# Performance work log

Hardware: AMD Instinct MI355X
Metric: run time of the kernel (lower is better)

Reference implementation:

```python
import jax, jax.numpy as jnp
import numpy as np
from jax import lax

MASK_RATE = 0.2
EPS = 1e-6
H, DK = 12, 64  # heads, per-head dim


def layer_norm(x, g, b):
    mu = jnp.mean(x, axis=-1, keepdims=True)
    var = jnp.mean(jnp.square(x - mu), axis=-1, keepdims=True)
    return (x - mu) * lax.rsqrt(var + EPS) * g + b


def setup_inputs() -> dict:
    key = jax.random.key(0)
    ks = jax.random.split(key, 24)
    B, T, S, D, F, L = 64, 131072, 256, 768, 3072, 2
    w = lambda k, shp: (jax.random.normal(k, shp, jnp.float32) * 0.02)
    inp = {
        "inputs": jax.random.normal(ks[0], (B, T, 1), jnp.float32),
        "randomness": jax.random.uniform(ks[1], (B * S, 3), jnp.float32),
        "perm": jax.random.permutation(ks[2], B * S).astype(jnp.int32),
        "conv_w": w(ks[3], (512, 1, D)),
        "conv_b": jnp.zeros((D,), jnp.float32),
        "pos_emb": w(ks[4], (300, D)),
        "mask_tok": w(ks[5], (D,)),
        "agg_tok": w(ks[6], (D,)),
        "wq": w(ks[7], (L, D, D)), "bq": jnp.zeros((L, D), jnp.float32),
        "wk": w(ks[8], (L, D, D)), "bk": jnp.zeros((L, D), jnp.float32),
        "wv": w(ks[9], (L, D, D)), "bv": jnp.zeros((L, D), jnp.float32),
        "wo": w(ks[10], (L, D, D)), "bo": jnp.zeros((L, D), jnp.float32),
        "ln1_g": jnp.ones((L, D), jnp.float32), "ln1_b": jnp.zeros((L, D), jnp.float32),
        "w1": w(ks[11], (L, D, F)), "b1": jnp.zeros((L, F), jnp.float32),
        "w2": w(ks[12], (L, F, D)), "b2": jnp.zeros((L, D), jnp.float32),
        "ln2_g": jnp.ones((L, D), jnp.float32), "ln2_b": jnp.zeros((L, D), jnp.float32),
    }
    return inp


def forward(inputs, randomness, perm, conv_w, conv_b, pos_emb, mask_tok, agg_tok,
            wq, bq, wk, bk, wv, bv, wo, bo, ln1_g, ln1_b, w1, b1, w2, b2, ln2_g, ln2_b):
    # waveform -> patches: Conv1D kernel=512 stride=512 valid
    x = lax.conv_general_dilated(inputs, conv_w, window_strides=(512,), padding='VALID',
                                 dimension_numbers=('NWC', 'WIO', 'NWC')) + conv_b
    B, S, D = x.shape
    embeddings = x
    # --- BERT-style random token masking (vectorized replacement of python loop) ---
    r0, r1, r2 = randomness[:, 0], randomness[:, 1], randomness[:, 2]
    sel = r0 <= MASK_RATE
    m = (sel & (r1 <= 0.8)).astype(x.dtype).reshape(B, S)
    rnd = (sel & (r1 > 0.8) & (r2 <= 0.5)).astype(x.dtype).reshape(B, S)
    nt = (sel & (r1 > 0.8) & (r2 > 0.5)).astype(x.dtype).reshape(B, S)
    flat = lax.stop_gradient(x.reshape(B * S, D))
    shuf = flat[perm].reshape(B, S, D)
    masked = (x * (1.0 - m - rnd)[:, :, None]
              + mask_tok[None, None, :] * m[:, :, None]
              + shuf * rnd[:, :, None])
    mask_pos = m + rnd + nt
    # positional embeddings + [AGG] token
    h = masked + pos_emb[:S][None, :, :]
    h = jnp.concatenate([jnp.broadcast_to(agg_tok, (B, 1, D)), h], axis=1)  # [B, S+1, D]
    scale = 1.0 / np.sqrt(DK).astype(np.float32)
    for l in range(wq.shape[0]):
        # post-norm transformer encoder layer
        q = (jnp.einsum('bsd,de->bse', h, wq[l]) + bq[l]).reshape(B, S + 1, H, DK)
        k = (jnp.einsum('bsd,de->bse', h, wk[l]) + bk[l]).reshape(B, S + 1, H, DK)
        v = (jnp.einsum('bsd,de->bse', h, wv[l]) + bv[l]).reshape(B, S + 1, H, DK)
        scores = jnp.einsum('bqhd,bkhd->bhqk', q, k) * scale
        attn = jax.nn.softmax(scores, axis=-1)
        o = jnp.einsum('bhqk,bkhd->bqhd', attn, v).reshape(B, S + 1, D)
        o = jnp.einsum('bsd,de->bse', o, wo[l]) + bo[l]
        h = layer_norm(h + o, ln1_g[l], ln1_b[l])
        f = jax.nn.gelu(jnp.einsum('bsd,df->bsf', h, w1[l]) + b1[l])
        f = jnp.einsum('bsf,fd->bsd', f, w2[l]) + b2[l]
        h = layer_norm(h + f, ln2_g[l], ln2_b[l])
    aggregated = h[:, 0, :]
    predictions = h[:, 1:, :]  # == predictions_1d (input already [B,S,D])
    return aggregated, predictions, mask_pos, embeddings


def reference(inputs, randomness, perm, conv_w, conv_b, pos_emb, mask_tok, agg_tok,
              wq, bq, wk, bk, wv, bv, wo, bo, ln1_g, ln1_b, w1, b1, w2, b2, ln2_g, ln2_b):
    return forward(inputs, randomness, perm, conv_w, conv_b, pos_emb, mask_tok, agg_tok,
                   wq, bq, wk, bk, wv, bv, wo, bo, ln1_g, ln1_b, w1, b1, w2, b2, ln2_g, ln2_b)
```

## Files before the change

### kernel.cpp

```cpp
#include <hip/hip_runtime.h>
#include <hip/hip_bf16.h>
#include <math.h>

#define BB 64
#define SS 256
#define SP 257
#define DD 768
#define FF 3072
#define HH 12
#define DKK 64
#define ROWS (BB*SP)
#define MPAD 16512
#define MCONV (BB*SS)
#define RB ((size_t)ROWS * DD)
#define PRB ((size_t)MPAD * DD)

typedef short bf16x8 __attribute__((ext_vector_type(8)));
typedef float f32x4 __attribute__((ext_vector_type(4)));
typedef unsigned short ushort8v __attribute__((ext_vector_type(8)));

__device__ __forceinline__ ushort f2bf(float x) {
    union { __hip_bfloat16 h; ushort u; } c;
    c.h = __float2bfloat16(x);
    return c.u;
}
__device__ __forceinline__ float bf2f(ushort u) {
    union { __hip_bfloat16 h; ushort u; } c;
    c.u = u;
    return __bfloat162float(c.h);
}

__device__ __forceinline__ float gelu_tanh_f(float x) {
    float x3 = x * x * x;
    float u = 0.7978845608028654f * (x + 0.044715f * x3);
    return 0.5f * x * (1.0f + tanhf(u));
}

__device__ __forceinline__ void gload16(const ushort* g, ushort* l) {
    __builtin_amdgcn_global_load_lds(
        (__attribute__((address_space(1))) void*)(g),
        (__attribute__((address_space(3))) void*)(l), 16, 0, 0);
}

template <bool IS_MAX>
__device__ __forceinline__ float blk_reduce(float v, float* red4) {
    #pragma unroll
    for (int o = 32; o > 0; o >>= 1) {
        float other = __shfl_down(v, o, 64);
        v = IS_MAX ? fmaxf(v, other) : (v + other);
    }
    __syncthreads();
    if ((threadIdx.x & 63) == 0) red4[threadIdx.x >> 6] = v;
    __syncthreads();
    if (IS_MAX) return fmaxf(fmaxf(red4[0], red4[1]), fmaxf(red4[2], red4[3]));
    return red4[0] + red4[1] + red4[2] + red4[3];
}

__global__ __launch_bounds__(256) void conv_in_bf_kernel(
    const float* __restrict__ in, ushort* __restrict__ out)
{
    const size_t i = ((size_t)blockIdx.x * 256 + threadIdx.x) * 4;
    float4 v = *reinterpret_cast<const float4*>(&in[i]);
    ushort4 o;
    o.x = f2bf(v.x); o.y = f2bf(v.y); o.z = f2bf(v.z); o.w = f2bf(v.w);
    *reinterpret_cast<ushort4*>(&out[i]) = o;
}

__global__ __launch_bounds__(256) void wt_kernel(
    const float* __restrict__ W, ushort* __restrict__ Wt, int K, int N)
{
    __shared__ float tile[32][33];
    const int k0 = blockIdx.x * 32, n0 = blockIdx.y * 32;
    const int t = threadIdx.x;
    {
        const int r = t >> 3, c4 = (t & 7) * 4;
        float4 v = *reinterpret_cast<const float4*>(&W[(size_t)(k0 + r) * N + n0 + c4]);
        tile[r][c4 + 0] = v.x; tile[r][c4 + 1] = v.y;
        tile[r][c4 + 2] = v.z; tile[r][c4 + 3] = v.w;
    }
    __syncthreads();
    {
        const int n = t >> 3, k4 = (t & 7) * 4;
        ushort4 o;
        o.x = f2bf(tile[k4 + 0][n]); o.y = f2bf(tile[k4 + 1][n]);
        o.z = f2bf(tile[k4 + 2][n]); o.w = f2bf(tile[k4 + 3][n]);
        *reinterpret_cast<ushort4*>(&Wt[(size_t)(n0 + n) * K + k0 + k4]) = o;
    }
}

template <bool C_BF16, bool GELU>
__global__ __launch_bounds__(256) void gemm128(
    const ushort* __restrict__ A, const ushort* __restrict__ Bt,
    const float* __restrict__ bias, void* __restrict__ Cp,
    int M, int N, int K)
{
    __shared__ ushort As[128 * 64];
    __shared__ ushort Bs[128 * 64];
    const int tid = threadIdx.x;
    const int lane = tid & 63, w = tid >> 6;
    const int wr = w & 1, wc = w >> 1;
    const int lg = lane >> 4, lr = lane & 15;
    const int row0 = blockIdx.y * 128, col0 = blockIdx.x * 128;

    f32x4 acc[4][4];
    #pragma unroll
    for (int m = 0; m < 4; ++m)
        #pragma unroll
        for (int n = 0; n < 4; ++n)
            acc[m][n] = (f32x4){0.f, 0.f, 0.f, 0.f};

    const int g_rowoff = w * 8 + (lane >> 3);
    const int g_colu   = (lane & 7) * 8;

    for (int k0 = 0; k0 < K; k0 += 64) {
        #pragma unroll
        for (int r = 0; r < 4; ++r) {
            const int row = r * 32 + g_rowoff;
            gload16(&A[(size_t)(row0 + row) * K + k0 + g_colu],
                    &As[r * 2048 + w * 512]);
            gload16(&Bt[(size_t)(col0 + row) * K + k0 + g_colu],
                    &Bs[r * 2048 + w * 512]);
        }
        __syncthreads();

        #pragma unroll
        for (int ks = 0; ks < 2; ++ks) {
            bf16x8 af[4], bf[4];
            #pragma unroll
            for (int m = 0; m < 4; ++m)
                af[m] = *reinterpret_cast<const bf16x8*>(
                    &As[(wr * 64 + m * 16 + lr) * 64 + ks * 32 + lg * 8]);
            #pragma unroll
            for (int n = 0; n < 4; ++n)
                bf[n] = *reinterpret_cast<const bf16x8*>(
                    &Bs[(wc * 64 + n * 16 + lr) * 64 + ks * 32 + lg * 8]);
            #pragma unroll
            for (int m = 0; m < 4; ++m)
                #pragma unroll
                for (int n = 0; n < 4; ++n)
                    acc[m][n] = __builtin_amdgcn_mfma_f32_16x16x32_bf16(
                        af[m], bf[n], acc[m][n], 0, 0, 0);
        }
        __syncthreads();
    }

    #pragma unroll
    for (int m = 0; m < 4; ++m) {
        #pragma unroll
        for (int n = 0; n < 4; ++n) {
            const int col = col0 + wc * 64 + n * 16 + lr;
            const float bcol = bias[col];
            #pragma unroll
            for (int j = 0; j < 4; ++j) {
                const int row = row0 + wr * 64 + m * 16 + lg * 4 + j;
                float v = acc[m][n][j] + bcol;
                if (GELU) v = gelu_tanh_f(v);
                if (C_BF16) ((ushort*)Cp)[(size_t)row * N + col] = f2bf(v);
                else        ((float*)Cp)[(size_t)row * N + col] = v;
            }
        }
    }
}

__global__ __launch_bounds__(256) void build_h_kernel(
    const float* __restrict__ emb, const float* __restrict__ rnd3,
    const int* __restrict__ perm, const float* __restrict__ pos_emb,
    const float* __restrict__ mask_tok, const float* __restrict__ agg_tok,
    float* __restrict__ h, ushort* __restrict__ hb, float* __restrict__ mask_pos)
{
    const int sf = blockIdx.x;
    const int b = blockIdx.y;
    const int t = threadIdx.x;
    const size_t ro = ((size_t)b * SP + sf) * DD;
    float* hrow = h + ro;
    ushort* hbrow = hb + ro;
    if (sf == 0) {
        #pragma unroll
        for (int i = 0; i < 3; ++i) {
            const float v = agg_tok[t + 256 * i];
            hrow[t + 256 * i] = v;
            hbrow[t + 256 * i] = f2bf(v);
        }
        return;
    }
    const int s = sf - 1;
    const int idx = b * SS + s;
    const float r0 = rnd3[idx * 3 + 0];
    const float r1 = rnd3[idx * 3 + 1];
    const float r2 = rnd3[idx * 3 + 2];
    const bool sel = (r0 <= 0.2f);
    const float m  = (sel && r1 <= 0.8f) ? 1.f : 0.f;
    const float rn = (sel && r1 > 0.8f && r2 <= 0.5f) ? 1.f : 0.f;
    const float nt = (sel && r1 > 0.8f && r2 > 0.5f) ? 1.f : 0.f;
    if (t == 0) mask_pos[idx] = m + rn + nt;
    const int p = perm[idx];
    const float* xrow = emb + (size_t)idx * DD;
    const float* srow = emb + (size_t)p * DD;
    const float keep = 1.f - m - rn;
    #pragma unroll
    for (int i = 0; i < 3; ++i) {
        const int c = t + 256 * i;
        const float v = xrow[c] * keep + mask_tok[c] * m + srow[c] * rn + pos_emb[s * DD + c];
        hrow[c] = v;
        hbrow[c] = f2bf(v);
    }
}

__global__ __launch_bounds__(256) void vt_kernel(
    const ushort* __restrict__ V, ushort* __restrict__ Vt)
{
    const int bh = blockIdx.x;
    const int b = bh / HH, h = bh % HH;
    const int t = threadIdx.x;
    __shared__ ushort tile[64][65];
    const size_t vtb = (size_t)bh * 64 * 288;
    const int d = t & 63, kk = t >> 6;
    const int kq = t & 63, dg = t >> 6;
    for (int kt = 0; kt < 5; ++kt) {
        #pragma unroll
        for (int i = 0; i < 16; ++i) {
            const int r = kk + 4 * i;
            const int kg = kt * 64 + r;
            tile[r][d] = (kg < SP) ? V[((size_t)b * SP + kg) * DD + h * 64 + d] : (ushort)0;
        }
        __syncthreads();
        #pragma unroll
        for (int i = 0; i < 16; ++i) {
            const int dd2 = dg + 4 * i;
            const int k = kt * 64 + kq;
            if (k < 288) Vt[vtb + (size_t)dd2 * 288 + k] = tile[kq][dd2];
        }
        __syncthreads();
    }
}

__global__ __launch_bounds__(256) void attn_mfma(
    const ushort* __restrict__ Q, const ushort* __restrict__ K,
    const ushort* __restrict__ Vt, ushort* __restrict__ O)
{
    const int h = blockIdx.x, b = blockIdx.y;
    const int t = threadIdx.x, lane = t & 63, w = t >> 6;
    const int lg = lane >> 4, lr = lane & 15;
    __shared__ ushort Pl[4][16][296];

    const size_t qkbase = ((size_t)b * SP) * DD + (size_t)h * DKK;
    const size_t vtbase = (size_t)(b * HH + h) * 64 * 288;

    #pragma unroll
    for (int i = 0; i < 4; ++i) Pl[w][lr][272 + lg * 4 + i] = 0;

    for (int p = 0; p < 5; ++p) {
        const int q0 = p * 64 + w * 16;
        const int qr = min(q0 + lr, SP - 1);
        bf16x8 aq0 = *reinterpret_cast<const bf16x8*>(&Q[qkbase + (size_t)qr * DD + lg * 8]);
        bf16x8 aq1 = *reinterpret_cast<const bf16x8*>(&Q[qkbase + (size_t)qr * DD + 32 + lg * 8]);

        f32x4 sc[17];
        #pragma unroll
        for (int n = 0; n < 17; ++n) {
            const int kr = min(n * 16 + lr, SP - 1);
            const ushort* kp = &K[qkbase + (size_t)kr * DD + lg * 8];
            bf16x8 bk0 = *reinterpret_cast<const bf16x8*>(kp);
            bf16x8 bk1 = *reinterpret_cast<const bf16x8*>(kp + 32);
            f32x4 a = (f32x4){0.f, 0.f, 0.f, 0.f};
            a = __builtin_amdgcn_mfma_f32_16x16x32_bf16(aq0, bk0, a, 0, 0, 0);
            a = __builtin_amdgcn_mfma_f32_16x16x32_bf16(aq1, bk1, a, 0, 0, 0);
            sc[n] = a;
        }

        float rmax[4] = {-1e30f, -1e30f, -1e30f, -1e30f};
        #pragma unroll
        for (int n = 0; n < 17; ++n) {
            const int kcol = n * 16 + lr;
            if (kcol >= SP) {
                sc[n] = (f32x4){-1e30f, -1e30f, -1e30f, -1e30f};
            } else {
                sc[n] *= 0.125f;
            }
            #pragma unroll
            for (int j = 0; j < 4; ++j) rmax[j] = fmaxf(rmax[j], sc[n][j]);
        }
        #pragma unroll
        for (int msk = 1; msk <= 8; msk <<= 1)
            #pragma unroll
            for (int j = 0; j < 4; ++j)
                rmax[j] = fmaxf(rmax[j], __shfl_xor(rmax[j], msk, 64));

        float rsum[4] = {0.f, 0.f, 0.f, 0.f};
        #pragma unroll
        for (int n = 0; n < 17; ++n) {
            #pragma unroll
            for (int j = 0; j < 4; ++j) {
                const float e = __expf(sc[n][j] - rmax[j]);
                rsum[j] += e;
                Pl[w][lg * 4 + j][n * 16 + lr] = f2bf(e);
            }
        }
        #pragma unroll
        for (int msk = 1; msk <= 8; msk <<= 1)
            #pragma unroll
            for (int j = 0; j < 4; ++j)
                rsum[j] += __shfl_xor(rsum[j], msk, 64);

        __syncthreads();

        f32x4 o[4];
        #pragma unroll
        for (int dn = 0; dn < 4; ++dn) o[dn] = (f32x4){0.f, 0.f, 0.f, 0.f};
        #pragma unroll
        for (int kb = 0; kb < 9; ++kb) {
            bf16x8 pa = *reinterpret_cast<const bf16x8*>(&Pl[w][lr][kb * 32 + lg * 8]);
            #pragma unroll
            for (int dn = 0; dn < 4; ++dn) {
                bf16x8 bv = *reinterpret_cast<const bf16x8*>(
                    &Vt[vtbase + (size_t)(dn * 16 + lr) * 288 + kb * 32 + lg * 8]);
                o[dn] = __builtin_amdgcn_mfma_f32_16x16x32_bf16(pa, bv, o[dn], 0, 0, 0);
            }
        }

        float rinv[4];
        #pragma unroll
        for (int j = 0; j < 4; ++j) rinv[j] = 1.f / rsum[j];
        #pragma unroll
        for (int dn = 0; dn < 4; ++dn) {
            #pragma unroll
            for (int j = 0; j < 4; ++j) {
                const int q = q0 + lg * 4 + j;
                if (q < SP)
                    O[qkbase + (size_t)q * DD + dn * 16 + lr] = f2bf(o[dn][j] * rinv[j]);
            }
        }
        __syncthreads();
    }
}

__global__ __launch_bounds__(256) void add_ln_kernel(
    float* __restrict__ h, ushort* __restrict__ hb, const ushort* __restrict__ r,
    const float* __restrict__ g, const float* __restrict__ bta)
{
    const int row = blockIdx.x;
    const int t = threadIdx.x;
    __shared__ float red4[4];
    float* hp = h + (size_t)row * DD;
    ushort* hbp = hb + (size_t)row * DD;
    const ushort* rp = r + (size_t)row * DD;
    const float x0 = hp[t]       + bf2f(rp[t]);
    const float x1 = hp[t + 256] + bf2f(rp[t + 256]);
    const float x2 = hp[t + 512] + bf2f(rp[t + 512]);
    const float s = blk_reduce<false>(x0 + x1 + x2, red4);
    const float mu = s * (1.f / 768.f);
    const float d0 = x0 - mu, d1 = x1 - mu, d2 = x2 - mu;
    const float v = blk_reduce<false>(d0 * d0 + d1 * d1 + d2 * d2, red4);
    const float inv = rsqrtf(v * (1.f / 768.f) + 1e-6f);
    const float y0 = d0 * inv * g[t]       + bta[t];
    const float y1 = d1 * inv * g[t + 256] + bta[t + 256];
    const float y2 = d2 * inv * g[t + 512] + bta[t + 512];
    hp[t]       = y0;  hbp[t]       = f2bf(y0);
    hp[t + 256] = y1;  hbp[t + 256] = f2bf(y1);
    hp[t + 512] = y2;  hbp[t + 512] = f2bf(y2);
}

__global__ __launch_bounds__(256) void out_copy_kernel(
    const float* __restrict__ h, float* __restrict__ agg, float* __restrict__ pred)
{
    const int sf = blockIdx.x;
    const int b = blockIdx.y;
    const int t = threadIdx.x;
    const float* hp = h + ((size_t)b * SP + sf) * DD;
    if (sf == 0) {
        #pragma unroll
        for (int i = 0; i < 3; ++i) agg[(size_t)b * DD + t + 256 * i] = hp[t + 256 * i];
    } else {
        float* pp = pred + ((size_t)(b * SS + sf - 1)) * DD;
        #pragma unroll
        for (int i = 0; i < 3; ++i) pp[t + 256 * i] = hp[t + 256 * i];
    }
}

extern "C" void kernel_launch(void* const* d_in, const int* in_sizes, int n_in,
                              void* d_out, int out_size, void* d_ws, size_t ws_size,
                              hipStream_t stream)
{
    const float* inputs   = (const float*)d_in[0];
    const float* rnd3     = (const float*)d_in[1];
    const int*   perm     = (const int*)d_in[2];
    const float* conv_w   = (const float*)d_in[3];
    const float* conv_b   = (const float*)d_in[4];
    const float* pos_emb  = (const float*)d_in[5];
    const float* mask_tok = (const float*)d_in[6];
    const float* agg_tok  = (const float*)d_in[7];
    const float* wq = (const float*)d_in[8];
    const float* bq = (const float*)d_in[9];
    const float* wk = (const float*)d_in[10];
    const float* bk = (const float*)d_in[11];
    const float* wv = (const float*)d_in[12];
    const float* bv = (const float*)d_in[13];
    const float* wo = (const float*)d_in[14];
    const float* bo = (const float*)d_in[15];
    const float* ln1_g = (const float*)d_in[16];
    const float* ln1_b = (const float*)d_in[17];
    const float* w1 = (const float*)d_in[18];
    const float* b1 = (const float*)d_in[19];
    const float* w2 = (const float*)d_in[20];
    const float* b2 = (const float*)d_in[21];
    const float* ln2_g = (const float*)d_in[22];
    const float* ln2_b = (const float*)d_in[23];

    float* out = (float*)d_out;
    float* agg_out  = out;
    float* pred_out = out + 49152;
    float* mask_out = out + 49152 + 12582912;
    float* emb_out  = out + 49152 + 12582912 + 16384;

    ushort* hb = (ushort*)pred_out;

    char* base = (char*)d_ws;
    float*  h    = (float*)base;
    ushort* qb   = (ushort*)(base + RB * 4);
    ushort* kb   = qb + PRB;
    ushort* vb   = kb + PRB;
    ushort* ob   = vb + PRB;
    ushort* mid  = qb;
    ushort* inbf = qb;
    ushort* vt   = ob + PRB;
    ushort* rbuf = vt;
    ushort* wptr = vt + (size_t)768 * 64 * 288;

    ushort* convT = wptr;                          wptr += (size_t)DD * 512;
    ushort* wqT[2]; ushort* wkT[2]; ushort* wvT[2]; ushort* woT[2];
    ushort* w1T[2]; ushort* w2T[2];
    for (int l = 0; l < 2; ++l) {
        wqT[l] = wptr; wptr += (size_t)DD * DD;
        wkT[l] = wptr; wptr += (size_t)DD * DD;
        wvT[l] = wptr; wptr += (size_t)DD * DD;
        woT[l] = wptr; wptr += (size_t)DD * DD;
        w1T[l] = wptr; wptr += (size_t)DD * FF;
        w2T[l] = wptr; wptr += (size_t)FF * DD;
    }

    const dim3 blk(256);

    conv_in_bf_kernel<<<dim3((MCONV * 512) / 1024), blk, 0, stream>>>(inputs, inbf);
    wt_kernel<<<dim3(512 / 32, DD / 32), blk, 0, stream>>>(conv_w, convT, 512, DD);
    for (int l = 0; l < 2; ++l) {
        wt_kernel<<<dim3(DD / 32, DD / 32), blk, 0, stream>>>(wq + (size_t)l*DD*DD, wqT[l], DD, DD);
        wt_kernel<<<dim3(DD / 32, DD / 32), blk, 0, stream>>>(wk + (size_t)l*DD*DD, wkT[l], DD, DD);
        wt_kernel<<<dim3(DD / 32, DD / 32), blk, 0, stream>>>(wv + (size_t)l*DD*DD, wvT[l], DD, DD);
        wt_kernel<<<dim3(DD / 32, DD / 32), blk, 0, stream>>>(wo + (size_t)l*DD*DD, woT[l], DD, DD);
        wt_kernel<<<dim3(DD / 32, FF / 32), blk, 0, stream>>>(w1 + (size_t)l*DD*FF, w1T[l], DD, FF);
        wt_kernel<<<dim3(FF / 32, DD / 32), blk, 0, stream>>>(w2 + (size_t)l*FF*DD, w2T[l], FF, DD);
    }

    gemm128<false, false><<<dim3(DD / 128, MCONV / 128), blk, 0, stream>>>(
        inbf, convT, conv_b, emb_out, MCONV, DD, 512);

    build_h_kernel<<<dim3(SP, BB), blk, 0, stream>>>(
        emb_out, rnd3, perm, pos_emb, mask_tok, agg_tok, h, hb, mask_out);

    for (int l = 0; l < 2; ++l) {
        gemm128<true, false><<<dim3(DD / 128, MPAD / 128), blk, 0, stream>>>(
            hb, wqT[l], bq + l * DD, qb, MPAD, DD, DD);
        gemm128<true, false><<<dim3(DD / 128, MPAD / 128), blk, 0, stream>>>(
            hb, wkT[l], bk + l * DD, kb, MPAD, DD, DD);
        gemm128<true, false><<<dim3(DD / 128, MPAD / 128), blk, 0, stream>>>(
            hb, wvT[l], bv + l * DD, vb, MPAD, DD, DD);

        vt_kernel<<<dim3(BB * HH), blk, 0, stream>>>(vb, vt);
        attn_mfma<<<dim3(HH, BB), blk, 0, stream>>>(qb, kb, vt, ob);

        gemm128<true, false><<<dim3(DD / 128, MPAD / 128), blk, 0, stream>>>(
            ob, woT[l], bo + l * DD, rbuf, MPAD, DD, DD);

        add_ln_kernel<<<dim3(ROWS), blk, 0, stream>>>(
            h, hb, rbuf, ln1_g + l * DD, ln1_b + l * DD);

        gemm128<true, true><<<dim3(FF / 128, MPAD / 128), blk, 0, stream>>>(
            hb, w1T[l], b1 + l * FF, mid, MPAD, FF, DD);
        gemm128<true, false><<<dim3(DD / 128, MPAD / 128), blk, 0, stream>>>(
            mid, w2T[l], b2 + l * DD, rbuf, MPAD, DD, FF);

        add_ln_kernel<<<dim3(ROWS), blk, 0, stream>>>(
            h, hb, rbuf, ln2_g + l * DD, ln2_b + l * DD);
    }

    out_copy_kernel<<<dim3(SP, BB), blk, 0, stream>>>(h, agg_out, pred_out);
}
```

Baseline: 1.599 ms.

## Pipeline GEMM K-loop with 4-slot LDS ring and XOR-swizzled tiles

Replaces the single-buffered 128x128 GEMM with a 4-stage LDS ring that prefetches three K=32 slices ahead. Each iteration waits on a partial vmcnt and a single barrier instead of two full syncs. LDS tiles are XOR-swizzled to avoid bank conflicts, K becomes a template parameter, launch bounds request 2 blocks per CU, and MFMA issue gets raised priority. GELU is rewritten in an exp-based sigmoid form, which is mathematically the same as the tanh form but may differ slightly in rounding.

```diff
diff --git a/kernel.cpp b/kernel.cpp
--- a/kernel.cpp
+++ b/kernel.cpp
@@ -30,10 +30,9 @@
     return __bfloat162float(c.h);
 }
 
-__device__ __forceinline__ float gelu_tanh_f(float x) {
-    float x3 = x * x * x;
-    float u = 0.7978845608028654f * (x + 0.044715f * x3);
-    return 0.5f * x * (1.0f + tanhf(u));
+__device__ __forceinline__ float gelu_fast(float x) {
+    const float u = x * (1.0f + 0.044715f * x * x);
+    return x / (1.0f + __expf(-1.5957691216057308f * u));
 }
 
 __device__ __forceinline__ void gload16(const ushort* g, ushort* l) {
@@ -88,14 +87,14 @@
     }
 }
 
-template <bool C_BF16, bool GELU>
-__global__ __launch_bounds__(256) void gemm128(
+template <int K, bool C_BF16, bool GELU>
+__global__ __launch_bounds__(256, 2) void gemm_pipe(
     const ushort* __restrict__ A, const ushort* __restrict__ Bt,
     const float* __restrict__ bias, void* __restrict__ Cp,
-    int M, int N, int K)
-{
-    __shared__ ushort As[128 * 64];
-    __shared__ ushort Bs[128 * 64];
+    int M, int N)
+{
+    constexpr int NT = K / 32;
+    __shared__ ushort lds[4][2][4096];
     const int tid = threadIdx.x;
     const int lane = tid & 63, w = tid >> 6;
     const int wr = w & 1, wc = w >> 1;
@@ -109,40 +108,65 @@
         for (int n = 0; n < 4; ++n)
             acc[m][n] = (f32x4){0.f, 0.f, 0.f, 0.f};
 
-    const int g_rowoff = w * 8 + (lane >> 3);
-    const int g_colu   = (lane & 7) * 8;
-
-    for (int k0 = 0; k0 < K; k0 += 64) {
-        #pragma unroll
-        for (int r = 0; r < 4; ++r) {
-            const int row = r * 32 + g_rowoff;
-            gload16(&A[(size_t)(row0 + row) * K + k0 + g_colu],
-                    &As[r * 2048 + w * 512]);
-            gload16(&Bt[(size_t)(col0 + row) * K + k0 + g_colu],
-                    &Bs[r * 2048 + w * 512]);
-        }
-        __syncthreads();
-
-        #pragma unroll
-        for (int ks = 0; ks < 2; ++ks) {
-            bf16x8 af[4], bf[4];
-            #pragma unroll
-            for (int m = 0; m < 4; ++m)
-                af[m] = *reinterpret_cast<const bf16x8*>(
-                    &As[(wr * 64 + m * 16 + lr) * 64 + ks * 32 + lg * 8]);
+    const int s_row0 = tid >> 2;
+    const int s_row1 = 64 + (tid >> 2);
+    const int kg0 = ((tid & 3) ^ (s_row0 & 3)) * 8;
+    const int kg1 = ((tid & 3) ^ (s_row1 & 3)) * 8;
+    const ushort* Ab = A + (size_t)row0 * K;
+    const ushort* Bb = Bt + (size_t)col0 * K;
+
+    auto STAGE = [&](int slot, int t) {
+        const int k0 = t * 32;
+        gload16(Ab + (size_t)s_row0 * K + k0 + kg0, &lds[slot][0][w * 512]);
+        gload16(Ab + (size_t)s_row1 * K + k0 + kg1, &lds[slot][0][2048 + w * 512]);
+        gload16(Bb + (size_t)s_row0 * K + k0 + kg0, &lds[slot][1][w * 512]);
+        gload16(Bb + (size_t)s_row1 * K + k0 + kg1, &lds[slot][1][2048 + w * 512]);
+    };
+
+    const int swz = (lg ^ (lr & 3)) * 8;
+
+    auto COMPUTE = [&](int slot) {
+        bf16x8 af[4], bfr[4];
+        #pragma unroll
+        for (int m = 0; m < 4; ++m)
+            af[m] = *reinterpret_cast<const bf16x8*>(
+                &lds[slot][0][(wr * 64 + m * 16 + lr) * 32 + swz]);
+        #pragma unroll
+        for (int n = 0; n < 4; ++n)
+            bfr[n] = *reinterpret_cast<const bf16x8*>(
+                &lds[slot][1][(wc * 64 + n * 16 + lr) * 32 + swz]);
+        __builtin_amdgcn_s_setprio(1);
+        #pragma unroll
+        for (int m = 0; m < 4; ++m)
             #pragma unroll
             for (int n = 0; n < 4; ++n)
-                bf[n] = *reinterpret_cast<const bf16x8*>(
-                    &Bs[(wc * 64 + n * 16 + lr) * 64 + ks * 32 + lg * 8]);
-            #pragma unroll
-            for (int m = 0; m < 4; ++m)
-                #pragma unroll
-                for (int n = 0; n < 4; ++n)
-                    acc[m][n] = __builtin_amdgcn_mfma_f32_16x16x32_bf16(
-                        af[m], bf[n], acc[m][n], 0, 0, 0);
-        }
-        __syncthreads();
-    }
+                acc[m][n] = __builtin_amdgcn_mfma_f32_16x16x32_bf16(
+                    af[m], bfr[n], acc[m][n], 0, 0, 0);
+        __builtin_amdgcn_s_setprio(0);
+    };
+
+    STAGE(0, 0); STAGE(1, 1); STAGE(2, 2);
+    asm volatile("s_waitcnt vmcnt(8)" ::: "memory");
+    __builtin_amdgcn_s_barrier();
+    asm volatile("" ::: "memory");
+
+    #pragma unroll 4
+    for (int t = 0; t < NT - 3; ++t) {
+        STAGE((t + 3) & 3, t + 3);
+        COMPUTE(t & 3);
+        asm volatile("s_waitcnt vmcnt(8)" ::: "memory");
+        __builtin_amdgcn_s_barrier();
+        asm volatile("" ::: "memory");
+    }
+    COMPUTE((NT - 3) & 3);
+    asm volatile("s_waitcnt vmcnt(4)" ::: "memory");
+    __builtin_amdgcn_s_barrier();
+    asm volatile("" ::: "memory");
+    COMPUTE((NT - 2) & 3);
+    asm volatile("s_waitcnt vmcnt(0)" ::: "memory");
+    __builtin_amdgcn_s_barrier();
+    asm volatile("" ::: "memory");
+    COMPUTE((NT - 1) & 3);
 
     #pragma unroll
     for (int m = 0; m < 4; ++m) {
@@ -154,7 +178,7 @@
             for (int j = 0; j < 4; ++j) {
                 const int row = row0 + wr * 64 + m * 16 + lg * 4 + j;
                 float v = acc[m][n][j] + bcol;
-                if (GELU) v = gelu_tanh_f(v);
+                if (GELU) v = gelu_fast(v);
                 if (C_BF16) ((ushort*)Cp)[(size_t)row * N + col] = f2bf(v);
                 else        ((float*)Cp)[(size_t)row * N + col] = v;
             }
@@ -451,33 +475,33 @@
         wt_kernel<<<dim3(FF / 32, DD / 32), blk, 0, stream>>>(w2 + (size_t)l*FF*DD, w2T[l], FF, DD);
     }
 
-    gemm128<false, false><<<dim3(DD / 128, MCONV / 128), blk, 0, stream>>>(
-        inbf, convT, conv_b, emb_out, MCONV, DD, 512);
+    gemm_pipe<512, false, false><<<dim3(DD / 128, MCONV / 128), blk, 0, stream>>>(
+        inbf, convT, conv_b, emb_out, MCONV, DD);
 
     build_h_kernel<<<dim3(SP, BB), blk, 0, stream>>>(
         emb_out, rnd3, perm, pos_emb, mask_tok, agg_tok, h, hb, mask_out);
 
     for (int l = 0; l < 2; ++l) {
-        gemm128<true, false><<<dim3(DD / 128, MPAD / 128), blk, 0, stream>>>(
-            hb, wqT[l], bq + l * DD, qb, MPAD, DD, DD);
-        gemm128<true, false><<<dim3(DD / 128, MPAD / 128), blk, 0, stream>>>(
-            hb, wkT[l], bk + l * DD, kb, MPAD, DD, DD);
-        gemm128<true, false><<<dim3(DD / 128, MPAD / 128), blk, 0, stream>>>(
-            hb, wvT[l], bv + l * DD, vb, MPAD, DD, DD);
+        gemm_pipe<768, true, false><<<dim3(DD / 128, MPAD / 128), blk, 0, stream>>>(
+            hb, wqT[l], bq + l * DD, qb, MPAD, DD);
+        gemm_pipe<768, true, false><<<dim3(DD / 128, MPAD / 128), blk, 0, stream>>>(
+            hb, wkT[l], bk + l * DD, kb, MPAD, DD);
+        gemm_pipe<768, true, false><<<dim3(DD / 128, MPAD / 128), blk, 0, stream>>>(
+            hb, wvT[l], bv + l * DD, vb, MPAD, DD);
 
         vt_kernel<<<dim3(BB * HH), blk, 0, stream>>>(vb, vt);
         attn_mfma<<<dim3(HH, BB), blk, 0, stream>>>(qb, kb, vt, ob);
 
-        gemm128<true, false><<<dim3(DD / 128, MPAD / 128), blk, 0, stream>>>(
-            ob, woT[l], bo + l * DD, rbuf, MPAD, DD, DD);
+        gemm_pipe<768, true, false><<<dim3(DD / 128, MPAD / 128), blk, 0, stream>>>(
+            ob, woT[l], bo + l * DD, rbuf, MPAD, DD);
 
         add_ln_kernel<<<dim3(ROWS), blk, 0, stream>>>(
             h, hb, rbuf, ln1_g + l * DD, ln1_b + l * DD);
 
-        gemm128<true, true><<<dim3(FF / 128, MPAD / 128), blk, 0, stream>>>(
-            hb, w1T[l], b1 + l * FF, mid, MPAD, FF, DD);
-        gemm128<true, false><<<dim3(DD / 128, MPAD / 128), blk, 0, stream>>>(
-            mid, w2T[l], b2 + l * DD, rbuf, MPAD, DD, FF);
+        gemm_pipe<768, true, true><<<dim3(FF / 128, MPAD / 128), blk, 0, stream>>>(
+            hb, w1T[l], b1 + l * FF, mid, MPAD, FF);
+        gemm_pipe<3072, true, false><<<dim3(DD / 128, MPAD / 128), blk, 0, stream>>>(
+            mid, w2T[l], b2 + l * DD, rbuf, MPAD, DD);
 
         add_ln_kernel<<<dim3(ROWS), blk, 0, stream>>>(
             h, hb, rbuf, ln2_g + l * DD, ln2_b + l * DD);
```

New measurement: 1.371 ms. 14.3% less time.
